# Performance work log

Measured on AMD Instinct MI355X. Metric: run time of the kernel, lower is better.

## Reference

```python
import jax, jax.numpy as jnp
import numpy as np

B, H, W, C = 16, 128, 128, 128
Wh = Ww = 8
SH = 4  # shift size
NH = 4  # heads
HD = C // NH
N = Wh * Ww
HID = 4 * C
EPS = 1e-3  # keras LayerNormalization default epsilon
SCALE = HD ** -0.5


def _rel_pos_index():
    coords = np.stack(np.meshgrid(np.arange(Wh), np.arange(Ww), indexing='ij'))  # (2,Wh,Ww)
    flat = coords.reshape(2, -1)
    rel = flat[:, :, None] - flat[:, None, :]  # (2,N,N)
    rel = rel.transpose(1, 2, 0) + np.array([Wh - 1, Ww - 1])
    rel = rel * np.array([2 * Ww - 1, 1])
    return rel.sum(-1).astype(np.int32)  # (N,N)


def _attn_mask():
    img = np.zeros((1, H, W, 1))
    h_sl = (slice(0, H - Wh), slice(H - Wh, H - SH), slice(H - SH, H))
    w_sl = (slice(0, W - Ww), slice(W - Ww, W - SH), slice(W - SH, W))
    cnt = 0
    for hs in h_sl:
        for ws in w_sl:
            img[:, hs, ws, :] = cnt
            cnt += 1
    mw = img.reshape(1, H // Wh, Wh, W // Ww, Ww, 1).transpose(0, 1, 3, 2, 4, 5).reshape(-1, N)
    am = mw[:, None, :] - mw[:, :, None]
    return np.where(am != 0, -100.0, 0.0).astype(np.float32)  # (nW,N,N)


def setup_inputs() -> dict:
    key = jax.random.key(0)
    ks = jax.random.split(key, 12)
    s = 0.02
    return {
        'x': jax.random.normal(ks[0], (B, H * W, C), jnp.float32),
        'w_qkv': jax.random.normal(ks[1], (C, 3 * C), jnp.float32) * s,
        'b_qkv': jnp.zeros((3 * C,), jnp.float32),
        'bias_table': jax.random.normal(ks[2], ((2 * Wh - 1) * (2 * Ww - 1), NH), jnp.float32) * s,
        'w_proj': jax.random.normal(ks[3], (C, C), jnp.float32) * s,
        'b_proj': jnp.zeros((C,), jnp.float32),
        'g1': jnp.ones((C,), jnp.float32),
        'be1': jnp.zeros((C,), jnp.float32),
        'w_fc1': jax.random.normal(ks[4], (C, HID), jnp.float32) * s,
        'b_fc1': jnp.zeros((HID,), jnp.float32),
        'w_fc2': jax.random.normal(ks[5], (HID, C), jnp.float32) * s,
        'b_fc2': jnp.zeros((C,), jnp.float32),
        'g2': jnp.ones((C,), jnp.float32),
        'be2': jnp.zeros((C,), jnp.float32),
        'rel_index': jnp.asarray(_rel_pos_index()),
        'attn_mask': jnp.asarray(_attn_mask()),
    }


def _ln(x, g, b):
    m = jnp.mean(x, -1, keepdims=True)
    v = jnp.mean(jnp.square(x - m), -1, keepdims=True)
    return (x - m) * jax.lax.rsqrt(v + EPS) * g + b


def _block(x, w_qkv, b_qkv, bias_table, w_proj, b_proj, g1, be1,
           w_fc1, b_fc1, w_fc2, b_fc2, g2, be2, rel_index, attn_mask):
    xi = x.reshape(B, H, W, C)
    xs = jnp.roll(xi, (-SH, -SH), axis=(1, 2))
    # window partition -> (B*nW, N, C)
    xw = xs.reshape(B, H // Wh, Wh, W // Ww, Ww, C).transpose(0, 1, 3, 2, 4, 5).reshape(-1, N, C)
    qkv = (xw @ w_qkv + b_qkv).reshape(-1, N, 3, NH, HD).transpose(2, 0, 3, 1, 4)
    q, k, v = qkv[0] * SCALE, qkv[1], qkv[2]
    attn = jnp.einsum('bhnd,bhmd->bhnm', q, k)  # (B*nW, NH, N, N)
    rpb = bias_table[rel_index.reshape(-1)].reshape(N, N, NH).transpose(2, 0, 1)
    attn = attn + rpb[None]
    nW = attn_mask.shape[0]
    attn = attn.reshape(-1, nW, NH, N, N) + attn_mask[None, :, None]
    attn = jax.nn.softmax(attn.reshape(-1, NH, N, N), axis=-1)
    out = jnp.einsum('bhnm,bhmd->bhnd', attn, v).transpose(0, 2, 1, 3).reshape(-1, N, C)
    out = out @ w_proj + b_proj
    # window reverse + unshift
    out = out.reshape(B, H // Wh, W // Ww, Wh, Ww, C).transpose(0, 1, 3, 2, 4, 5).reshape(B, H, W, C)
    out = jnp.roll(out, (SH, SH), axis=(1, 2)).reshape(B, H * W, C)
    # NOTE: this module applies norm AFTER the sublayers (post-norm residual)
    x = x + _ln(out, g1, be1)
    h = jax.nn.gelu(x @ w_fc1 + b_fc1, approximate=False) @ w_fc2 + b_fc2
    x = x + _ln(h, g2, be2)
    return x


def reference(x, w_qkv, b_qkv, bias_table, w_proj, b_proj, g1, be1,
              w_fc1, b_fc1, w_fc2, b_fc2, g2, be2, rel_index, attn_mask):
    return _block(x, w_qkv, b_qkv, bias_table, w_proj, b_proj, g1, be1,
                  w_fc1, b_fc1, w_fc2, b_fc2, g2, be2, rel_index, attn_mask)
```

## Files before the change

### kernel.cpp

```cpp
#include <hip/hip_runtime.h>
#include <hip/hip_bf16.h>
#include <math.h>

typedef unsigned short u16;
typedef unsigned int   u32;

typedef __bf16 bf16x8 __attribute__((ext_vector_type(8)));
typedef float  f32x4  __attribute__((ext_vector_type(4)));
#define MFMA_B16 __builtin_amdgcn_mfma_f32_16x16x32_bf16

__device__ __forceinline__ u16 f2b(float f) {
    union { float f; u32 i; } v; v.f = f;
    u32 x = v.i;
    u32 r = x + 0x7fffu + ((x >> 16) & 1u);
    return (u16)(r >> 16);
}
__device__ __forceinline__ u32 pk2(float a, float b) {
    return (u32)f2b(a) | ((u32)f2b(b) << 16);
}
__device__ __forceinline__ bf16x8 pk8(float4 f0, float4 f1) {
    union { u32 u[4]; bf16x8 v; } cv;
    cv.u[0] = pk2(f0.x, f0.y); cv.u[1] = pk2(f0.z, f0.w);
    cv.u[2] = pk2(f1.x, f1.y); cv.u[3] = pk2(f1.z, f1.w);
    return cv.v;
}

__device__ __forceinline__ float gelu_fast(float v) {
    const float z = v * (1.5957691f + 0.07135486f * v * v);
    return v * __builtin_amdgcn_rcpf(1.0f + __expf(-z));
}

__device__ __forceinline__ int qk_idx(int row, int d) {
    return row * 32 + (d ^ (((row >> 1) & 3) << 3));
}
__device__ __forceinline__ int p_idx(int row, int col) {
    return row * 64 + (col ^ ((row & 7) << 3));
}

#define SCALE_ 0.17677669529663687f
#define EPS_   1e-3f


__global__ __launch_bounds__(256) void swin_prep(
    const float* __restrict__ w_qkv, const float* __restrict__ w_proj,
    const float* __restrict__ w_fc1, const float* __restrict__ w_fc2,
    const float* __restrict__ bias_table, const int* __restrict__ rel_index,
    const float* __restrict__ attn_mask,
    u16* __restrict__ wqkvT, u16* __restrict__ wprojT,
    u16* __restrict__ w1T, u16* __restrict__ w2T, float* __restrict__ rpbm)
{
    const int idx = blockIdx.x * 256 + threadIdx.x;
    if (idx < 49152) {
        const int o = idx >> 7, c = idx & 127;
        wqkvT[idx] = f2b(w_qkv[c * 384 + o]);
    } else if (idx < 65536) {
        const int i2 = idx - 49152;
        const int o = i2 >> 7, c = i2 & 127;
        wprojT[i2] = f2b(w_proj[c * 128 + o]);
    } else if (idx < 131072) {
        const int i2 = idx - 65536;
        const int o = i2 >> 7, c = i2 & 127;
        w1T[i2] = f2b(w_fc1[c * 512 + o]);
    } else if (idx < 196608) {
        const int i2 = idx - 131072;
        const int o = i2 >> 9, u = i2 & 511;
        w2T[i2] = f2b(w_fc2[u * 128 + o]);
    } else if (idx < 262144) {
        const int i2 = idx - 196608;
        const int cls = i2 >> 14, rem = i2 & 16383;
        const int h = rem >> 12, ij = rem & 4095;
        const int widx = ((cls & 2) ? 240 : 0) + ((cls & 1) ? 15 : 0);
        rpbm[i2] = bias_table[rel_index[ij] * 4 + h] + attn_mask[widx * 4096 + ij];
    }
}

#define QA_OFF  0
#define KA_OFF  8192
#define VA_OFF  16384
#define PA_OFF  0
#define AO_OFF  0
#define X2F_OFF 4352

__global__ __launch_bounds__(256, 3) void swin_attn_mfma(
    const float* __restrict__ x, const u16* __restrict__ wqkvT, const float* __restrict__ b_qkv,
    const u16* __restrict__ wprojT, const float* __restrict__ b_proj,
    const float* __restrict__ g1, const float* __restrict__ be1,
    const float* __restrict__ rpbm, float* __restrict__ x1out)
{
    __shared__ __align__(16) u16 sm[25600];
    const int tid  = threadIdx.x;
    const int w    = tid >> 6;
    const int lane = tid & 63;
    const int l15  = lane & 15;
    const int quad = lane >> 4;
    const int win  = blockIdx.x;
    const int b = win >> 8, wr = (win >> 4) & 15, wc = win & 15;

    size_t rowb[4];
    #pragma unroll
    for (int mi = 0; mi < 4; mi++) {
        const int t  = mi * 16 + l15;
        const int hh = (wr * 8 + (t >> 3) + 4) & 127;
        const int ww = (wc * 8 + (t & 7) + 4) & 127;
        rowb[mi] = ((size_t)((b * 128 + hh) * 128 + ww)) * 128;
    }

    {
        f32x4 acc[6][4];
        #pragma unroll
        for (int n = 0; n < 6; n++) {
            const float bq = b_qkv[w * 96 + n * 16 + l15];
            #pragma unroll
            for (int mi = 0; mi < 4; mi++) acc[n][mi] = (f32x4){bq, bq, bq, bq};
        }
        #pragma unroll
        for (int ks = 0; ks < 4; ks++) {
            bf16x8 a[4], bb[6];
            #pragma unroll
            for (int mi = 0; mi < 4; mi++) {
                const float4 f0 = *(const float4*)(x + rowb[mi] + ks * 32 + quad * 8);
                const float4 f1 = *(const float4*)(x + rowb[mi] + ks * 32 + quad * 8 + 4);
                a[mi] = pk8(f0, f1);
            }
            #pragma unroll
            for (int n = 0; n < 6; n++)
                bb[n] = *(const bf16x8*)(wqkvT + (size_t)(w * 96 + n * 16 + l15) * 128 + ks * 32 + quad * 8);
            #pragma unroll
            for (int n = 0; n < 6; n++)
                #pragma unroll
                for (int mi = 0; mi < 4; mi++)
                    acc[n][mi] = MFMA_B16(a[mi], bb[n], acc[n][mi], 0, 0, 0);
        }
        #pragma unroll
        for (int n = 0; n < 6; n++) {
            const int o = w * 96 + n * 16 + l15;
            const int s = o >> 7, h = (o >> 5) & 3, d = o & 31;
            #pragma unroll
            for (int mi = 0; mi < 4; mi++) {
                if (s < 2) {
                    const int base = (s ? KA_OFF : QA_OFF) + h * 2048;
                    const float sc = s ? 1.0f : SCALE_;
                    #pragma unroll
                    for (int r = 0; r < 4; r++) {
                        const int row = mi * 16 + quad * 4 + r;
                        sm[base + qk_idx(row, d)] = f2b(acc[n][mi][r] * sc);
                    }
                } else {
                    const int t0 = mi * 16 + quad * 4;
                    const u32 w0 = pk2(acc[n][mi][0], acc[n][mi][1]);
                    const u32 w1 = pk2(acc[n][mi][2], acc[n][mi][3]);
                    *(uint2*)(sm + VA_OFF + h * 2304 + d * 72 + t0) = make_uint2(w0, w1);
                }
            }
        }
    }
    __syncthreads();

    float sinv[4][4];
    {
        const int h = w;
        const float* rb = rpbm + (size_t)((((wr == 15) ? 2 : 0) | ((wc == 15) ? 1 : 0)) * 4 + h) * 4096;
        f32x4 S[4][4];
        #pragma unroll
        for (int mi = 0; mi < 4; mi++)
            #pragma unroll
            for (int ni = 0; ni < 4; ni++)
                #pragma unroll
                for (int r = 0; r < 4; r++)
                    S[mi][ni][r] = rb[(mi * 16 + quad * 4 + r) * 64 + ni * 16 + l15];
        bf16x8 aq[4], bk[4];
        #pragma unroll
        for (int mi = 0; mi < 4; mi++)
            aq[mi] = *(const bf16x8*)(sm + QA_OFF + h * 2048 + qk_idx(mi * 16 + l15, quad * 8));
        #pragma unroll
        for (int ni = 0; ni < 4; ni++)
            bk[ni] = *(const bf16x8*)(sm + KA_OFF + h * 2048 + qk_idx(ni * 16 + l15, quad * 8));
        #pragma unroll
        for (int mi = 0; mi < 4; mi++)
            #pragma unroll
            for (int ni = 0; ni < 4; ni++)
                S[mi][ni] = MFMA_B16(aq[mi], bk[ni], S[mi][ni], 0, 0, 0);
        #pragma unroll
        for (int mi = 0; mi < 4; mi++) {
            #pragma unroll
            for (int r = 0; r < 4; r++) {
                float m0 = fmaxf(fmaxf(S[mi][0][r], S[mi][1][r]), fmaxf(S[mi][2][r], S[mi][3][r]));
                m0 = fmaxf(m0, __shfl_xor(m0, 1));
                m0 = fmaxf(m0, __shfl_xor(m0, 2));
                m0 = fmaxf(m0, __shfl_xor(m0, 4));
                m0 = fmaxf(m0, __shfl_xor(m0, 8));
                float s0 = 0.0f;
                #pragma unroll
                for (int ni = 0; ni < 4; ni++) {
                    const float e = __expf(S[mi][ni][r] - m0);
                    S[mi][ni][r] = e;
                    s0 += e;
                }
                s0 += __shfl_xor(s0, 1);
                s0 += __shfl_xor(s0, 2);
                s0 += __shfl_xor(s0, 4);
                s0 += __shfl_xor(s0, 8);
                sinv[mi][r] = __builtin_amdgcn_rcpf(s0);
            }
        }
        __syncthreads();

        #pragma unroll
        for (int mi = 0; mi < 4; mi++)
            #pragma unroll
            for (int ni = 0; ni < 4; ni++)
                #pragma unroll
                for (int r = 0; r < 4; r++)
                    sm[PA_OFF + h * 4096 + p_idx(mi * 16 + quad * 4 + r, ni * 16 + l15)] = f2b(S[mi][ni][r]);

        f32x4 O[4][2];
        #pragma unroll
        for (int mi = 0; mi < 4; mi++)
            #pragma unroll
            for (int ni = 0; ni < 2; ni++) O[mi][ni] = (f32x4){0.f, 0.f, 0.f, 0.f};
        #pragma unroll
        for (int ks = 0; ks < 2; ks++) {
            bf16x8 ap[4], bv[2];
            #pragma unroll
            for (int mi = 0; mi < 4; mi++)
                ap[mi] = *(const bf16x8*)(sm + PA_OFF + h * 4096 + p_idx(mi * 16 + l15, ks * 32 + quad * 8));
            #pragma unroll
            for (int ni = 0; ni < 2; ni++)
                bv[ni] = *(const bf16x8*)(sm + VA_OFF + h * 2304 + (ni * 16 + l15) * 72 + ks * 32 + quad * 8);
            #pragma unroll
            for (int mi = 0; mi < 4; mi++)
                #pragma unroll
                for (int ni = 0; ni < 2; ni++)
                    O[mi][ni] = MFMA_B16(ap[mi], bv[ni], O[mi][ni], 0, 0, 0);
        }
        __syncthreads();

        #pragma unroll
        for (int mi = 0; mi < 4; mi++)
            #pragma unroll
            for (int ni = 0; ni < 2; ni++)
                #pragma unroll
                for (int r = 0; r < 4; r++)
                    sm[AO_OFF + (mi * 16 + quad * 4 + r) * 136 + h * 32 + ni * 16 + l15]
                        = f2b(O[mi][ni][r] * sinv[mi][r]);
    }
    __syncthreads();

    {
        f32x4 X2[4][2];
        #pragma unroll
        for (int ni = 0; ni < 2; ni++) {
            const float bp = b_proj[w * 32 + ni * 16 + l15];
            #pragma unroll
            for (int mi = 0; mi < 4; mi++) X2[mi][ni] = (f32x4){bp, bp, bp, bp};
        }
        #pragma unroll
        for (int ks = 0; ks < 4; ks++) {
            bf16x8 aa[4], bw[2];
            #pragma unroll
            for (int mi = 0; mi < 4; mi++)
                aa[mi] = *(const bf16x8*)(sm + AO_OFF + (mi * 16 + l15) * 136 + ks * 32 + quad * 8);
            #pragma unroll
            for (int ni = 0; ni < 2; ni++)
                bw[ni] = *(const bf16x8*)(wprojT + (size_t)(w * 32 + ni * 16 + l15) * 128 + ks * 32 + quad * 8);
            #pragma unroll
            for (int mi = 0; mi < 4; mi++)
                #pragma unroll
                for (int ni = 0; ni < 2; ni++)
                    X2[mi][ni] = MFMA_B16(aa[mi], bw[ni], X2[mi][ni], 0, 0, 0);
        }
        float* X2f = (float*)sm + X2F_OFF;
        #pragma unroll
        for (int mi = 0; mi < 4; mi++)
            #pragma unroll
            for (int ni = 0; ni < 2; ni++)
                #pragma unroll
                for (int r = 0; r < 4; r++)
                    X2f[(mi * 16 + quad * 4 + r) * 132 + w * 32 + ni * 16 + l15] = X2[mi][ni][r];
    }
    __syncthreads();

    {
        const int t = tid >> 2, part = tid & 3;
        const float* Xr = (const float*)sm + X2F_OFF + t * 132 + part * 32;
        float4 xr[8];
        float s1 = 0.f, s2 = 0.f;
        #pragma unroll
        for (int k = 0; k < 8; k++) {
            xr[k] = *(const float4*)(Xr + k * 4);
            s1 += xr[k].x + xr[k].y + xr[k].z + xr[k].w;
            s2 += xr[k].x * xr[k].x + xr[k].y * xr[k].y
                + xr[k].z * xr[k].z + xr[k].w * xr[k].w;
        }
        s1 += __shfl_xor(s1, 1); s1 += __shfl_xor(s1, 2);
        s2 += __shfl_xor(s2, 1); s2 += __shfl_xor(s2, 2);
        const float m  = s1 * 0.0078125f;
        const float vr = fmaxf(s2 * 0.0078125f - m * m, 0.f);
        const float rs = rsqrtf(vr + EPS_);
        const int hh = (wr * 8 + (t >> 3) + 4) & 127;
        const int ww = (wc * 8 + (t & 7) + 4) & 127;
        const size_t g = ((size_t)((b * 128 + hh) * 128 + ww)) * 128 + part * 32;
        #pragma unroll
        for (int k = 0; k < 8; k++) {
            const int c4 = k * 4;
            const float4 xv = *(const float4*)(x + g + c4);
            const float4 gv = *(const float4*)(g1 + part * 32 + c4);
            const float4 bv = *(const float4*)(be1 + part * 32 + c4);
            float4 o;
            o.x = xv.x + (xr[k].x - m) * rs * gv.x + bv.x;
            o.y = xv.y + (xr[k].y - m) * rs * gv.y + bv.y;
            o.z = xv.z + (xr[k].z - m) * rs * gv.z + bv.z;
            o.w = xv.w + (xr[k].w - m) * rs * gv.w + bv.w;
            *(float4*)(x1out + g + c4) = o;
        }
    }
}

#define HB_OFF 8704

__global__ __launch_bounds__(256, 4) void swin_mlp_mfma(
    float* __restrict__ x1io, const u16* __restrict__ w1T, const float* __restrict__ b_fc1,
    const u16* __restrict__ w2T, const float* __restrict__ b_fc2,
    const float* __restrict__ g2, const float* __restrict__ be2)
{
    __shared__ __align__(16) u16 sm[17408];
    const int tid  = threadIdx.x;
    const int w    = tid >> 6;
    const int lane = tid & 63;
    const int l15  = lane & 15;
    const int quad = lane >> 4;
    const size_t base = (size_t)blockIdx.x * 8192;

    for (int e = tid * 8; e < 8192; e += 2048) {
        const int t = e >> 7, c = e & 127;
        const float4 f0 = *(const float4*)(x1io + base + e);
        const float4 f1 = *(const float4*)(x1io + base + e + 4);
        union { bf16x8 v; uint4 u; } cv; cv.v = pk8(f0, f1);
        *(uint4*)(sm + t * 136 + c) = cv.u;
    }
    __syncthreads();

    f32x4 acc2[2][4];
    #pragma unroll
    for (int ni = 0; ni < 2; ni++) {
        const float bb = b_fc2[w * 32 + ni * 16 + l15];
        #pragma unroll
        for (int mi = 0; mi < 4; mi++) acc2[ni][mi] = (f32x4){bb, bb, bb, bb};
    }

    for (int ch = 0; ch < 4; ch++) {
        f32x4 a1[2][4];
        #pragma unroll
        for (int ni = 0; ni < 2; ni++) {
            const float bb = b_fc1[ch * 128 + (w * 2 + ni) * 16 + l15];
            #pragma unroll
            for (int mi = 0; mi < 4; mi++) a1[ni][mi] = (f32x4){bb, bb, bb, bb};
        }
        #pragma unroll
        for (int ks = 0; ks < 4; ks++) {
            bf16x8 af[4], bf[2];
            #pragma unroll
            for (int mi = 0; mi < 4; mi++)
                af[mi] = *(const bf16x8*)(sm + (mi * 16 + l15) * 136 + ks * 32 + quad * 8);
            #pragma unroll
            for (int ni = 0; ni < 2; ni++)
                bf[ni] = *(const bf16x8*)(w1T + (size_t)(ch * 128 + (w * 2 + ni) * 16 + l15) * 128 + ks * 32 + quad * 8);
            #pragma unroll
            for (int ni = 0; ni < 2; ni++)
                #pragma unroll
                for (int mi = 0; mi < 4; mi++)
                    a1[ni][mi] = MFMA_B16(af[mi], bf[ni], a1[ni][mi], 0, 0, 0);
        }
        #pragma unroll
        for (int ni = 0; ni < 2; ni++)
            #pragma unroll
            for (int mi = 0; mi < 4; mi++)
                #pragma unroll
                for (int r = 0; r < 4; r++) {
                    const float v = gelu_fast(a1[ni][mi][r]);
                    sm[HB_OFF + (mi * 16 + quad * 4 + r) * 136 + (w * 2 + ni) * 16 + l15] = f2b(v);
                }
        __syncthreads();
        #pragma unroll
        for (int ks = 0; ks < 4; ks++) {
            bf16x8 ah[4], bh[2];
            #pragma unroll
            for (int mi = 0; mi < 4; mi++)
                ah[mi] = *(const bf16x8*)(sm + HB_OFF + (mi * 16 + l15) * 136 + ks * 32 + quad * 8);
            #pragma unroll
            for (int ni = 0; ni < 2; ni++)
                bh[ni] = *(const bf16x8*)(w2T + (size_t)(w * 32 + ni * 16 + l15) * 512 + ch * 128 + ks * 32 + quad * 8);
            #pragma unroll
            for (int ni = 0; ni < 2; ni++)
                #pragma unroll
                for (int mi = 0; mi < 4; mi++)
                    acc2[ni][mi] = MFMA_B16(ah[mi], bh[ni], acc2[ni][mi], 0, 0, 0);
        }
        __syncthreads();
    }

    {
        float* X3 = (float*)sm;
        #pragma unroll
        for (int ni = 0; ni < 2; ni++)
            #pragma unroll
            for (int mi = 0; mi < 4; mi++)
                #pragma unroll
                for (int r = 0; r < 4; r++)
                    X3[(mi * 16 + quad * 4 + r) * 132 + w * 32 + ni * 16 + l15] = acc2[ni][mi][r];
    }
    __syncthreads();

    {
        const int t = tid >> 2, part = tid & 3;
        const float* Xr = (const float*)sm + t * 132 + part * 32;
        float4 xr[8];
        float s1 = 0.f, s2 = 0.f;
        #pragma unroll
        for (int k = 0; k < 8; k++) {
            xr[k] = *(const float4*)(Xr + k * 4);
            s1 += xr[k].x + xr[k].y + xr[k].z + xr[k].w;
            s2 += xr[k].x * xr[k].x + xr[k].y * xr[k].y
                + xr[k].z * xr[k].z + xr[k].w * xr[k].w;
        }
        s1 += __shfl_xor(s1, 1); s1 += __shfl_xor(s1, 2);
        s2 += __shfl_xor(s2, 1); s2 += __shfl_xor(s2, 2);
        const float m  = s1 * 0.0078125f;
        const float vr = fmaxf(s2 * 0.0078125f - m * m, 0.f);
        const float rs = rsqrtf(vr + EPS_);
        const size_t g = base + t * 128 + part * 32;
        #pragma unroll
        for (int k = 0; k < 8; k++) {
            const int c4 = k * 4;
            const float4 xv = *(const float4*)(x1io + g + c4);
            const float4 gv = *(const float4*)(g2 + part * 32 + c4);
            const float4 bv = *(const float4*)(be2 + part * 32 + c4);
            float4 o;
            o.x = xv.x + (xr[k].x - m) * rs * gv.x + bv.x;
            o.y = xv.y + (xr[k].y - m) * rs * gv.y + bv.y;
            o.z = xv.z + (xr[k].z - m) * rs * gv.z + bv.z;
            o.w = xv.w + (xr[k].w - m) * rs * gv.w + bv.w;
            *(float4*)(x1io + g + c4) = o;
        }
    }
}

extern "C" void kernel_launch(void* const* d_in, const int* in_sizes, int n_in,
                              void* d_out, int out_size, void* d_ws, size_t ws_size,
                              hipStream_t stream) {
    const float* x         = (const float*)d_in[0];
    const float* w_qkv     = (const float*)d_in[1];
    const float* b_qkv     = (const float*)d_in[2];
    const float* bias_tab  = (const float*)d_in[3];
    const float* w_proj    = (const float*)d_in[4];
    const float* b_proj    = (const float*)d_in[5];
    const float* g1        = (const float*)d_in[6];
    const float* be1       = (const float*)d_in[7];
    const float* w_fc1     = (const float*)d_in[8];
    const float* b_fc1     = (const float*)d_in[9];
    const float* w_fc2     = (const float*)d_in[10];
    const float* b_fc2     = (const float*)d_in[11];
    const float* g2        = (const float*)d_in[12];
    const float* be2       = (const float*)d_in[13];
    const int* rel_index   = (const int*)d_in[14];
    const float* attn_mask = (const float*)d_in[15];

    char* ws = (char*)d_ws;
    u16*   wqkvT  = (u16*)ws;
    u16*   wprojT = (u16*)(ws + 98304);
    u16*   w1T    = (u16*)(ws + 131072);
    u16*   w2T    = (u16*)(ws + 262144);
    float* rpbm   = (float*)(ws + 393216);

    float* x1 = (float*)d_out;

    swin_prep<<<1024, 256, 0, stream>>>(w_qkv, w_proj, w_fc1, w_fc2,
                                        bias_tab, rel_index, attn_mask,
                                        wqkvT, wprojT, w1T, w2T, rpbm);
    swin_attn_mfma<<<4096, 256, 0, stream>>>(x, wqkvT, b_qkv, wprojT, b_proj,
                                             g1, be1, rpbm, x1);
    swin_mlp_mfma<<<4096, 256, 0, stream>>>(x1, w1T, b_fc1, w2T, b_fc2, g2, be2);
}
```

Before: 663.7 us.

## Give each wave full rows so LayerNorm reduces in registers without LDS

The projection and both MLP GEMMs are re-partitioned so that each wave computes 16 rows across all 128 output columns, instead of a 64x32 tile. LayerNorm statistics can then be reduced with lane shuffles in registers, which removes the fp32 LDS staging buffer and its block barriers. The MLP hidden activations move to a per-wave LDS slice, which drops the per-chunk __syncthreads. In exchange, every wave now streams the whole weight matrices from global memory or cache, and the epilogue stores are scalar and narrower. The MLP residual is also read back from the bf16 LDS copy instead of the fp32 input, which lowers accuracy.

```diff
diff --git a/kernel.cpp b/kernel.cpp
--- a/kernel.cpp
+++ b/kernel.cpp
@@ -14,6 +14,9 @@
     u32 x = v.i;
     u32 r = x + 0x7fffu + ((x >> 16) & 1u);
     return (u16)(r >> 16);
+}
+__device__ __forceinline__ float b2f(u16 u) {
+    union { u32 i; float f; } v; v.i = ((u32)u) << 16; return v.f;
 }
 __device__ __forceinline__ u32 pk2(float a, float b) {
     return (u32)f2b(a) | ((u32)f2b(b) << 16);
@@ -79,7 +82,6 @@
 #define VA_OFF  16384
 #define PA_OFF  0
 #define AO_OFF  0
-#define X2F_OFF 4352
 
 __global__ __launch_bounds__(256, 3) void swin_attn_mfma(
     const float* __restrict__ x, const u16* __restrict__ wqkvT, const float* __restrict__ b_qkv,
@@ -247,76 +249,62 @@
     __syncthreads();
 
     {
-        f32x4 X2[4][2];
-        #pragma unroll
-        for (int ni = 0; ni < 2; ni++) {
-            const float bp = b_proj[w * 32 + ni * 16 + l15];
-            #pragma unroll
-            for (int mi = 0; mi < 4; mi++) X2[mi][ni] = (f32x4){bp, bp, bp, bp};
+        size_t gb[4];
+        float xres[4][8];
+        #pragma unroll
+        for (int r = 0; r < 4; r++) {
+            const int t  = w * 16 + quad * 4 + r;
+            const int hh = (wr * 8 + (t >> 3) + 4) & 127;
+            const int ww = (wc * 8 + (t & 7) + 4) & 127;
+            gb[r] = ((size_t)((b * 128 + hh) * 128 + ww)) * 128;
+            #pragma unroll
+            for (int ni = 0; ni < 8; ni++)
+                xres[r][ni] = x[gb[r] + ni * 16 + l15];
+        }
+        float g1v[8], be1v[8];
+        #pragma unroll
+        for (int ni = 0; ni < 8; ni++) {
+            g1v[ni]  = g1[ni * 16 + l15];
+            be1v[ni] = be1[ni * 16 + l15];
+        }
+
+        f32x4 X2[8];
+        #pragma unroll
+        for (int ni = 0; ni < 8; ni++) {
+            const float bp = b_proj[ni * 16 + l15];
+            X2[ni] = (f32x4){bp, bp, bp, bp};
         }
         #pragma unroll
         for (int ks = 0; ks < 4; ks++) {
-            bf16x8 aa[4], bw[2];
-            #pragma unroll
-            for (int mi = 0; mi < 4; mi++)
-                aa[mi] = *(const bf16x8*)(sm + AO_OFF + (mi * 16 + l15) * 136 + ks * 32 + quad * 8);
-            #pragma unroll
-            for (int ni = 0; ni < 2; ni++)
-                bw[ni] = *(const bf16x8*)(wprojT + (size_t)(w * 32 + ni * 16 + l15) * 128 + ks * 32 + quad * 8);
-            #pragma unroll
-            for (int mi = 0; mi < 4; mi++)
-                #pragma unroll
-                for (int ni = 0; ni < 2; ni++)
-                    X2[mi][ni] = MFMA_B16(aa[mi], bw[ni], X2[mi][ni], 0, 0, 0);
-        }
-        float* X2f = (float*)sm + X2F_OFF;
-        #pragma unroll
-        for (int mi = 0; mi < 4; mi++)
-            #pragma unroll
-            for (int ni = 0; ni < 2; ni++)
-                #pragma unroll
-                for (int r = 0; r < 4; r++)
-                    X2f[(mi * 16 + quad * 4 + r) * 132 + w * 32 + ni * 16 + l15] = X2[mi][ni][r];
-    }
-    __syncthreads();
-
-    {
-        const int t = tid >> 2, part = tid & 3;
-        const float* Xr = (const float*)sm + X2F_OFF + t * 132 + part * 32;
-        float4 xr[8];
-        float s1 = 0.f, s2 = 0.f;
-        #pragma unroll
-        for (int k = 0; k < 8; k++) {
-            xr[k] = *(const float4*)(Xr + k * 4);
-            s1 += xr[k].x + xr[k].y + xr[k].z + xr[k].w;
-            s2 += xr[k].x * xr[k].x + xr[k].y * xr[k].y
-                + xr[k].z * xr[k].z + xr[k].w * xr[k].w;
-        }
-        s1 += __shfl_xor(s1, 1); s1 += __shfl_xor(s1, 2);
-        s2 += __shfl_xor(s2, 1); s2 += __shfl_xor(s2, 2);
-        const float m  = s1 * 0.0078125f;
-        const float vr = fmaxf(s2 * 0.0078125f - m * m, 0.f);
-        const float rs = rsqrtf(vr + EPS_);
-        const int hh = (wr * 8 + (t >> 3) + 4) & 127;
-        const int ww = (wc * 8 + (t & 7) + 4) & 127;
-        const size_t g = ((size_t)((b * 128 + hh) * 128 + ww)) * 128 + part * 32;
-        #pragma unroll
-        for (int k = 0; k < 8; k++) {
-            const int c4 = k * 4;
-            const float4 xv = *(const float4*)(x + g + c4);
-            const float4 gv = *(const float4*)(g1 + part * 32 + c4);
-            const float4 bv = *(const float4*)(be1 + part * 32 + c4);
-            float4 o;
-            o.x = xv.x + (xr[k].x - m) * rs * gv.x + bv.x;
-            o.y = xv.y + (xr[k].y - m) * rs * gv.y + bv.y;
-            o.z = xv.z + (xr[k].z - m) * rs * gv.z + bv.z;
-            o.w = xv.w + (xr[k].w - m) * rs * gv.w + bv.w;
-            *(float4*)(x1out + g + c4) = o;
-        }
-    }
-}
-
-#define HB_OFF 8704
+            const bf16x8 aa = *(const bf16x8*)(sm + AO_OFF + (w * 16 + l15) * 136 + ks * 32 + quad * 8);
+            #pragma unroll
+            for (int ni = 0; ni < 8; ni++) {
+                const bf16x8 bw = *(const bf16x8*)(wprojT + (size_t)(ni * 16 + l15) * 128 + ks * 32 + quad * 8);
+                X2[ni] = MFMA_B16(aa, bw, X2[ni], 0, 0, 0);
+            }
+        }
+        #pragma unroll
+        for (int r = 0; r < 4; r++) {
+            float s1 = 0.f, s2 = 0.f;
+            #pragma unroll
+            for (int ni = 0; ni < 8; ni++) {
+                const float v = X2[ni][r];
+                s1 += v; s2 += v * v;
+            }
+            s1 += __shfl_xor(s1, 1); s1 += __shfl_xor(s1, 2);
+            s1 += __shfl_xor(s1, 4); s1 += __shfl_xor(s1, 8);
+            s2 += __shfl_xor(s2, 1); s2 += __shfl_xor(s2, 2);
+            s2 += __shfl_xor(s2, 4); s2 += __shfl_xor(s2, 8);
+            const float m  = s1 * 0.0078125f;
+            const float vr = fmaxf(s2 * 0.0078125f - m * m, 0.f);
+            const float rs = rsqrtf(vr + EPS_);
+            #pragma unroll
+            for (int ni = 0; ni < 8; ni++)
+                x1out[gb[r] + ni * 16 + l15] =
+                    xres[r][ni] + (X2[ni][r] - m) * rs * g1v[ni] + be1v[ni];
+        }
+    }
+}
 
 __global__ __launch_bounds__(256, 4) void swin_mlp_mfma(
     float* __restrict__ x1io, const u16* __restrict__ w1T, const float* __restrict__ b_fc1,
@@ -340,107 +328,77 @@
     }
     __syncthreads();
 
-    f32x4 acc2[2][4];
+    u16* hw = sm + 8704 + w * 2176;
+
+    f32x4 acc2[8];
     #pragma unroll
-    for (int ni = 0; ni < 2; ni++) {
-        const float bb = b_fc2[w * 32 + ni * 16 + l15];
-        #pragma unroll
-        for (int mi = 0; mi < 4; mi++) acc2[ni][mi] = (f32x4){bb, bb, bb, bb};
+    for (int ni = 0; ni < 8; ni++) {
+        const float bb = b_fc2[ni * 16 + l15];
+        acc2[ni] = (f32x4){bb, bb, bb, bb};
     }
 
     for (int ch = 0; ch < 4; ch++) {
-        f32x4 a1[2][4];
-        #pragma unroll
-        for (int ni = 0; ni < 2; ni++) {
-            const float bb = b_fc1[ch * 128 + (w * 2 + ni) * 16 + l15];
-            #pragma unroll
-            for (int mi = 0; mi < 4; mi++) a1[ni][mi] = (f32x4){bb, bb, bb, bb};
+        f32x4 a1[8];
+        #pragma unroll
+        for (int ni = 0; ni < 8; ni++) {
+            const float bb = b_fc1[ch * 128 + ni * 16 + l15];
+            a1[ni] = (f32x4){bb, bb, bb, bb};
         }
         #pragma unroll
         for (int ks = 0; ks < 4; ks++) {
-            bf16x8 af[4], bf[2];
-            #pragma unroll
-            for (int mi = 0; mi < 4; mi++)
-                af[mi] = *(const bf16x8*)(sm + (mi * 16 + l15) * 136 + ks * 32 + quad * 8);
-            #pragma unroll
-            for (int ni = 0; ni < 2; ni++)
-                bf[ni] = *(const bf16x8*)(w1T + (size_t)(ch * 128 + (w * 2 + ni) * 16 + l15) * 128 + ks * 32 + quad * 8);
-            #pragma unroll
-            for (int ni = 0; ni < 2; ni++)
-                #pragma unroll
-                for (int mi = 0; mi < 4; mi++)
-                    a1[ni][mi] = MFMA_B16(af[mi], bf[ni], a1[ni][mi], 0, 0, 0);
-        }
-        #pragma unroll
-        for (int ni = 0; ni < 2; ni++)
-            #pragma unroll
-            for (int mi = 0; mi < 4; mi++)
-                #pragma unroll
-                for (int r = 0; r < 4; r++) {
-                    const float v = gelu_fast(a1[ni][mi][r]);
-                    sm[HB_OFF + (mi * 16 + quad * 4 + r) * 136 + (w * 2 + ni) * 16 + l15] = f2b(v);
-                }
-        __syncthreads();
+            const bf16x8 af = *(const bf16x8*)(sm + (w * 16 + l15) * 136 + ks * 32 + quad * 8);
+            #pragma unroll
+            for (int ni = 0; ni < 8; ni++) {
+                const bf16x8 bf = *(const bf16x8*)(w1T + (size_t)(ch * 128 + ni * 16 + l15) * 128 + ks * 32 + quad * 8);
+                a1[ni] = MFMA_B16(af, bf, a1[ni], 0, 0, 0);
+            }
+        }
+        #pragma unroll
+        for (int ni = 0; ni < 8; ni++)
+            #pragma unroll
+            for (int r = 0; r < 4; r++)
+                hw[(quad * 4 + r) * 136 + ni * 16 + l15] = f2b(gelu_fast(a1[ni][r]));
         #pragma unroll
         for (int ks = 0; ks < 4; ks++) {
-            bf16x8 ah[4], bh[2];
-            #pragma unroll
-            for (int mi = 0; mi < 4; mi++)
-                ah[mi] = *(const bf16x8*)(sm + HB_OFF + (mi * 16 + l15) * 136 + ks * 32 + quad * 8);
-            #pragma unroll
-            for (int ni = 0; ni < 2; ni++)
-                bh[ni] = *(const bf16x8*)(w2T + (size_t)(w * 32 + ni * 16 + l15) * 512 + ch * 128 + ks * 32 + quad * 8);
-            #pragma unroll
-            for (int ni = 0; ni < 2; ni++)
-                #pragma unroll
-                for (int mi = 0; mi < 4; mi++)
-                    acc2[ni][mi] = MFMA_B16(ah[mi], bh[ni], acc2[ni][mi], 0, 0, 0);
-        }
-        __syncthreads();
+            const bf16x8 ah = *(const bf16x8*)(hw + l15 * 136 + ks * 32 + quad * 8);
+            #pragma unroll
+            for (int ni = 0; ni < 8; ni++) {
+                const bf16x8 bh = *(const bf16x8*)(w2T + (size_t)(ni * 16 + l15) * 512 + ch * 128 + ks * 32 + quad * 8);
+                acc2[ni] = MFMA_B16(ah, bh, acc2[ni], 0, 0, 0);
+            }
+        }
     }
 
     {
-        float* X3 = (float*)sm;
-        #pragma unroll
-        for (int ni = 0; ni < 2; ni++)
-            #pragma unroll
-            for (int mi = 0; mi < 4; mi++)
-                #pragma unroll
-                for (int r = 0; r < 4; r++)
-                    X3[(mi * 16 + quad * 4 + r) * 132 + w * 32 + ni * 16 + l15] = acc2[ni][mi][r];
-    }
-    __syncthreads();
-
-    {
-        const int t = tid >> 2, part = tid & 3;
-        const float* Xr = (const float*)sm + t * 132 + part * 32;
-        float4 xr[8];
-        float s1 = 0.f, s2 = 0.f;
-        #pragma unroll
-        for (int k = 0; k < 8; k++) {
-            xr[k] = *(const float4*)(Xr + k * 4);
-            s1 += xr[k].x + xr[k].y + xr[k].z + xr[k].w;
-            s2 += xr[k].x * xr[k].x + xr[k].y * xr[k].y
-                + xr[k].z * xr[k].z + xr[k].w * xr[k].w;
-        }
-        s1 += __shfl_xor(s1, 1); s1 += __shfl_xor(s1, 2);
-        s2 += __shfl_xor(s2, 1); s2 += __shfl_xor(s2, 2);
-        const float m  = s1 * 0.0078125f;
-        const float vr = fmaxf(s2 * 0.0078125f - m * m, 0.f);
-        const float rs = rsqrtf(vr + EPS_);
-        const size_t g = base + t * 128 + part * 32;
-        #pragma unroll
-        for (int k = 0; k < 8; k++) {
-            const int c4 = k * 4;
-            const float4 xv = *(const float4*)(x1io + g + c4);
-            const float4 gv = *(const float4*)(g2 + part * 32 + c4);
-            const float4 bv = *(const float4*)(be2 + part * 32 + c4);
-            float4 o;
-            o.x = xv.x + (xr[k].x - m) * rs * gv.x + bv.x;
-            o.y = xv.y + (xr[k].y - m) * rs * gv.y + bv.y;
-            o.z = xv.z + (xr[k].z - m) * rs * gv.z + bv.z;
-            o.w = xv.w + (xr[k].w - m) * rs * gv.w + bv.w;
-            *(float4*)(x1io + g + c4) = o;
+        float g2v[8], be2v[8];
+        #pragma unroll
+        for (int ni = 0; ni < 8; ni++) {
+            g2v[ni]  = g2[ni * 16 + l15];
+            be2v[ni] = be2[ni * 16 + l15];
+        }
+        #pragma unroll
+        for (int r = 0; r < 4; r++) {
+            float s1 = 0.f, s2 = 0.f;
+            #pragma unroll
+            for (int ni = 0; ni < 8; ni++) {
+                const float v = acc2[ni][r];
+                s1 += v; s2 += v * v;
+            }
+            s1 += __shfl_xor(s1, 1); s1 += __shfl_xor(s1, 2);
+            s1 += __shfl_xor(s1, 4); s1 += __shfl_xor(s1, 8);
+            s2 += __shfl_xor(s2, 1); s2 += __shfl_xor(s2, 2);
+            s2 += __shfl_xor(s2, 4); s2 += __shfl_xor(s2, 8);
+            const float m  = s1 * 0.0078125f;
+            const float vr = fmaxf(s2 * 0.0078125f - m * m, 0.f);
+            const float rs = rsqrtf(vr + EPS_);
+            const int row = w * 16 + quad * 4 + r;
+            const size_t g = base + (size_t)row * 128;
+            #pragma unroll
+            for (int ni = 0; ni < 8; ni++) {
+                const int c = ni * 16 + l15;
+                const float xv = b2f(sm[row * 136 + c]);
+                x1io[g + c] = xv + (acc2[ni][r] - m) * rs * g2v[ni] + be2v[ni];
+            }
         }
     }
 }
```

Measured after the change: 922.5 us. 1.39x slower.
